# Performance work log

Hardware: AMD Instinct MI355X
Metric: run time of the kernel (lower is better)

Reference implementation:

```python
import jax, jax.numpy as jnp
import numpy as np

B, T, P = 4, 512, 3584          # batch, new tokens per seq, cached tokens per seq
D_MODEL, H, KH, DH = 2048, 16, 4, 128
N_REP = H // KH
MAX_SEQ = 4096
ROPE_BASE = 1e6
EPS = 1e-6


def _rmsnorm(t, w):
    # t: [..., DH]
    var = jnp.mean(t * t, axis=-1, keepdims=True)
    return t * jax.lax.rsqrt(var + EPS) * w


def _rope(t, positions):
    # t: [N, heads, DH], positions: [N] int
    half = DH // 2
    inv_freq = (1.0 / ROPE_BASE) ** (2.0 * jnp.arange(half, dtype=jnp.float32) / DH)
    theta = positions.astype(jnp.float32)[:, None] * inv_freq[None, :]   # [N, half]
    theta = jnp.concatenate([theta, theta], axis=-1)                      # [N, DH]
    sin = jnp.sin(theta)[:, None, :]
    cos = jnp.cos(theta)[:, None, :]
    x1, x2 = jnp.split(t, 2, axis=-1)
    rot = jnp.concatenate([-x2, x1], axis=-1)
    return cos * t + sin * rot


def setup_inputs() -> dict:
    key = jax.random.key(0)
    ks = jax.random.split(key, 9)
    N = B * T
    x = jax.random.normal(ks[0], (N, D_MODEL), dtype=jnp.float32)
    k_cache = jax.random.normal(ks[1], (B, KH, P, DH), dtype=jnp.float32)
    v_cache = jax.random.normal(ks[2], (B, KH, P, DH), dtype=jnp.float32)
    s = 1.0 / np.sqrt(D_MODEL)
    w_q = jax.random.normal(ks[3], (H * DH, D_MODEL), dtype=jnp.float32) * s
    w_k = jax.random.normal(ks[4], (KH * DH, D_MODEL), dtype=jnp.float32) * s
    w_v = jax.random.normal(ks[5], (KH * DH, D_MODEL), dtype=jnp.float32) * s
    w_o = jax.random.normal(ks[6], (D_MODEL, H * DH), dtype=jnp.float32) * s
    q_norm_w = jnp.ones((DH,), dtype=jnp.float32)
    k_norm_w = jnp.ones((DH,), dtype=jnp.float32)
    # each sequence's new tokens occupy absolute positions [P, P+T)
    positions = jnp.tile(P + jnp.arange(T, dtype=jnp.int32), B)  # [B*T]
    return {"x": x, "k_cache": k_cache, "v_cache": v_cache,
            "w_q": w_q, "w_k": w_k, "w_v": w_v, "w_o": w_o,
            "q_norm_w": q_norm_w, "k_norm_w": k_norm_w,
            "positions": positions}


def reference(x, k_cache, v_cache, w_q, w_k, w_v, w_o, q_norm_w, k_norm_w, positions):
    N = x.shape[0]
    # QKV projections (no bias)
    q = (x @ w_q.T).reshape(N, H, DH)
    k = (x @ w_k.T).reshape(N, KH, DH)
    v = (x @ w_v.T).reshape(N, KH, DH)
    # per-head RMSNorm then RoPE at absolute positions
    q = _rope(_rmsnorm(q, q_norm_w), positions)
    k = _rope(_rmsnorm(k, k_norm_w), positions)
    # assemble full KV: cached (pre-rotated) past + new tokens
    k_new = k.reshape(B, T, KH, DH).transpose(0, 2, 1, 3)   # [B,KH,T,DH]
    v_new = v.reshape(B, T, KH, DH).transpose(0, 2, 1, 3)
    k_full = jnp.concatenate([k_cache, k_new], axis=2)       # [B,KH,P+T,DH]
    v_full = jnp.concatenate([v_cache, v_new], axis=2)
    # GQA: repeat each kv head n_rep times
    k_rep = jnp.repeat(k_full, N_REP, axis=1)                # [B,H,S,DH]
    v_rep = jnp.repeat(v_full, N_REP, axis=1)
    q4 = q.reshape(B, T, H, DH).transpose(0, 2, 1, 3)        # [B,H,T,DH]
    scale = 1.0 / jnp.sqrt(jnp.float32(DH))
    scores = jnp.einsum('bhtd,bhsd->bhts', q4, k_rep) * scale  # [B,H,T,P+T]
    # right-bottom causal mask: q_pos = P + t, kv_pos = s
    q_pos = P + jnp.arange(T)
    kv_pos = jnp.arange(P + T)
    mask = q_pos[:, None] >= kv_pos[None, :]
    scores = jnp.where(mask[None, None], scores, -jnp.inf)
    attn = jax.nn.softmax(scores, axis=-1)
    out = jnp.einsum('bhts,bhsd->bhtd', attn, v_rep)          # [B,H,T,DH]
    out = out.transpose(0, 2, 1, 3).reshape(N, H * DH)
    return out @ w_o.T
```

## Files before the change

kernel.cpp:

```cpp
#include <hip/hip_runtime.h>
#include <hip/hip_bf16.h>
#include <stdint.h>

#define B_   4
#define T_   512
#define P_   3584
#define S_   4096
#define H_   16
#define KH_  4
#define DM_  2048
#define DH_  128
#define NTOK 2048
#define NCHUNK 3
#define NTC  43
#define NROWS 32768

typedef __attribute__((ext_vector_type(8)))  short          bf16x8;
typedef __attribute__((ext_vector_type(4)))  float          f32x4;
typedef __attribute__((ext_vector_type(16))) float          f32x16;
typedef __attribute__((ext_vector_type(4)))  float          f4v;
typedef __attribute__((ext_vector_type(4)))  unsigned short us4v;

__device__ __forceinline__ unsigned short f2bf(float x) {
    union { float f; unsigned u; } v; v.f = x;
    unsigned r = v.u + 0x7FFFu + ((v.u >> 16) & 1u);
    return (unsigned short)(r >> 16);
}
__device__ __forceinline__ float bf2f(unsigned short b) {
    union { unsigned u; float f; } v; v.u = ((unsigned)b) << 16; return v.f;
}
__device__ __forceinline__ unsigned pkbf(float a, float b) {
    __hip_bfloat162 h = __float22bfloat162_rn(float2{a, b});
    union { __hip_bfloat162 h; unsigned u; } cv; cv.h = h; return cv.u;
}

#define GLDS16(gp, lp) __builtin_amdgcn_global_load_lds( \
    (const __attribute__((address_space(1))) void*)(gp), \
    (__attribute__((address_space(3))) void*)(lp), 16, 0, 0)

__global__ __launch_bounds__(256) void convert_all(
    const float* __restrict__ x,  const float* __restrict__ wq,
    const float* __restrict__ wk, const float* __restrict__ wv,
    const float* __restrict__ wo, const float* __restrict__ kc,
    unsigned short* __restrict__ xb,   unsigned short* __restrict__ wqkvb,
    unsigned short* __restrict__ wob,  unsigned short* __restrict__ kfull)
{
    const long total = 5505024;
    for (long i = (long)blockIdx.x * 256 + threadIdx.x; i < total;
         i += (long)gridDim.x * 256) {
        const f4v* src; us4v* dst; long s4, d4;
        if (i < 1048576)      { src=(const f4v*)x;  dst=(us4v*)xb;              s4=i;         d4=s4; }
        else if (i < 2097152) { src=(const f4v*)wq; dst=(us4v*)wqkvb;           s4=i-1048576; d4=s4; }
        else if (i < 2359296) { src=(const f4v*)wk; dst=(us4v*)(wqkvb+4194304); s4=i-2097152; d4=s4; }
        else if (i < 2621440) { src=(const f4v*)wv; dst=(us4v*)(wqkvb+5242880); s4=i-2359296; d4=s4; }
        else if (i < 3670016) { src=(const f4v*)wo; dst=(us4v*)wob;             s4=i-2621440; d4=s4; }
        else                  { s4=i-3670016; long bk=s4/114688;
                                d4=bk*131072+(s4-bk*114688);
                                src=(const f4v*)kc; dst=(us4v*)kfull; }
        f4v v = src[s4];
        us4v o; o[0]=f2bf(v[0]); o[1]=f2bf(v[1]); o[2]=f2bf(v[2]); o[3]=f2bf(v[3]);
        dst[d4] = o;
    }
}

__global__ __launch_bounds__(256) void vcache_transpose(
    const float* __restrict__ vc, unsigned short* __restrict__ vT)
{
    __shared__ unsigned short tile[64][65];
    const int bk = blockIdx.z;
    const int st = blockIdx.x;
    const int dt = blockIdx.y;
    const float* src = vc + ((size_t)bk * P_ + st * 64) * DH_ + dt * 64;
    const int tq = threadIdx.x & 15;
    const int ts = threadIdx.x >> 4;
    #pragma unroll
    for (int i = 0; i < 4; ++i) {
        const int si = ts + i * 16;
        f4v v = *(const f4v*)(src + (size_t)si * DH_ + tq * 4);
        tile[si][tq*4+0] = f2bf(v[0]); tile[si][tq*4+1] = f2bf(v[1]);
        tile[si][tq*4+2] = f2bf(v[2]); tile[si][tq*4+3] = f2bf(v[3]);
    }
    __syncthreads();
    unsigned short* dst = vT + ((size_t)bk * DH_ + dt * 64) * S_ + st * 64;
    const int sq = threadIdx.x & 15;
    const int td = threadIdx.x >> 4;
    #pragma unroll
    for (int i = 0; i < 4; ++i) {
        const int di = td + i * 16;
        us4v o;
        o[0] = tile[sq*4+0][di]; o[1] = tile[sq*4+1][di];
        o[2] = tile[sq*4+2][di]; o[3] = tile[sq*4+3][di];
        *(us4v*)(dst + (size_t)di * S_ + sq * 4) = o;
    }
}

__global__ __launch_bounds__(256) void gemm_bt(
    const unsigned short* __restrict__ A, const unsigned short* __restrict__ Bw,
    void* __restrict__ C, int M, int N, int K, int obf16)
{
    __shared__ short As[2][128 * 32];
    __shared__ short Bs[2][128 * 32];
    const int tid = threadIdx.x, lane = tid & 63, w = tid >> 6;
    const int nbn = N >> 7;
    const int bm = blockIdx.x / nbn, bn = blockIdx.x % nbn;
    const int m0 = bm << 7, n0 = bn << 7;
    const int wm = w >> 1, wn = w & 1;

    f32x4 acc[4][4];
    #pragma unroll
    for (int i = 0; i < 4; ++i)
        #pragma unroll
        for (int j = 0; j < 4; ++j)
            #pragma unroll
            for (int r = 0; r < 4; ++r) acc[i][j][r] = 0.f;

    const int arow = lane >> 2;
    const int acol = (lane & 3) << 3;

    auto stage = [&](int buf, int k0) {
        #pragma unroll
        for (int cc = 0; cc < 2; ++cc) {
            const int c = 2 * w + cc;
            GLDS16(A  + (size_t)(m0 + c * 16 + arow) * K + k0 + acol, &As[buf][c * 512]);
            GLDS16(Bw + (size_t)(n0 + c * 16 + arow) * K + k0 + acol, &Bs[buf][c * 512]);
        }
    };

    stage(0, 0);
    __syncthreads();

    const int nk = K >> 5;
    const int fr = lane & 15, fk = (lane >> 4) << 3;
    for (int t = 0; t < nk; ++t) {
        const int buf = t & 1;
        if (t + 1 < nk) stage(buf ^ 1, (t + 1) << 5);
        bf16x8 a[4], b[4];
        #pragma unroll
        for (int i = 0; i < 4; ++i)
            a[i] = *(const bf16x8*)&As[buf][(wm * 64 + i * 16 + fr) * 32 + fk];
        #pragma unroll
        for (int j = 0; j < 4; ++j)
            b[j] = *(const bf16x8*)&Bs[buf][(wn * 64 + j * 16 + fr) * 32 + fk];
        #pragma unroll
        for (int i = 0; i < 4; ++i)
            #pragma unroll
            for (int j = 0; j < 4; ++j)
                acc[i][j] = __builtin_amdgcn_mfma_f32_16x16x32_bf16(a[i], b[j], acc[i][j], 0, 0, 0);
        __syncthreads();
    }

    const int er = lane >> 4, ec = lane & 15;
    #pragma unroll
    for (int i = 0; i < 4; ++i)
        #pragma unroll
        for (int j = 0; j < 4; ++j)
            #pragma unroll
            for (int r = 0; r < 4; ++r) {
                const int row = m0 + wm * 64 + i * 16 + er * 4 + r;
                const int col = n0 + wn * 64 + j * 16 + ec;
                if (obf16) ((unsigned short*)C)[(size_t)row * N + col] = f2bf(acc[i][j][r]);
                else       ((float*)C)[(size_t)row * N + col] = acc[i][j][r];
            }
}

__global__ __launch_bounds__(64) void norm_rope(
    const unsigned short* __restrict__ qkv, const float* __restrict__ qw,
    const float* __restrict__ kw,  const int* __restrict__ pos,
    unsigned short* __restrict__ Qb, unsigned short* __restrict__ Kf,
    unsigned short* __restrict__ VT)
{
    const int task = blockIdx.x;
    const int n = task / 24, idx = task % 24;
    const int lane = threadIdx.x;
    const int b = n >> 9, t = n & 511;

    if (idx >= 20) {
        const int kh = idx - 20;
        const unsigned short* src = qkv + (size_t)n * 3072 + 2560 + kh * 128;
        unsigned short* dstT = VT + (size_t)(b * KH_ + kh) * DH_ * S_ + (P_ + t);
        dstT[(size_t)lane * S_]        = src[lane];
        dstT[(size_t)(lane + 64) * S_] = src[lane + 64];
        return;
    }
    const bool isq = idx < 16;
    const int hh = isq ? idx : (idx - 16);
    const unsigned short* src = qkv + (size_t)n * 3072 + (isq ? hh * 128 : 2048 + hh * 128);
    const float* wn_ = isq ? qw : kw;
    float x0 = bf2f(src[lane]), x1 = bf2f(src[lane + 64]);
    float ss = x0 * x0 + x1 * x1;
    #pragma unroll
    for (int m = 1; m < 64; m <<= 1) ss += __shfl_xor(ss, m);
    const float rinv = rsqrtf(ss * (1.0f / 128.0f) + 1e-6f);
    float y0 = x0 * rinv * wn_[lane];
    float y1 = x1 * rinv * wn_[lane + 64];
    const float fr = __expf(-(float)lane * (13.815510557964274f / 64.0f));
    const float th = (float)pos[n] * fr;
    float sn, cs; sincosf(th, &sn, &cs);
    float o0 = cs * y0 - sn * y1;
    float o1 = cs * y1 + sn * y0;
    unsigned short* dst;
    if (isq) {
        o0 *= 0.08838834764831845f; o1 *= 0.08838834764831845f;
        dst = Qb + ((size_t)(b * H_ + hh) * T_ + t) * DH_;
    } else {
        dst = Kf + ((size_t)(b * KH_ + hh) * S_ + P_ + t) * DH_;
    }
    dst[lane]      = f2bf(o0);
    dst[lane + 64] = f2bf(o1);
}

__global__ __launch_bounds__(256, 3) void attn(
    const unsigned short* __restrict__ Qb, const unsigned short* __restrict__ Kf,
    const unsigned short* __restrict__ VT, unsigned short* __restrict__ op0,
    unsigned short* __restrict__ op1, unsigned short* __restrict__ op2,
    float2* __restrict__ ml)
{
    __shared__ short Ks[2][32 * 128];
    __shared__ short Vs[2][128 * 32];

    const int tid = threadIdx.x, lane = tid & 63, w = tid >> 6;
    const int c = blockIdx.x >> 8;
    const int rest = blockIdx.x & 255;
    const int qt = rest & 3;
    const int bh = rest >> 2;
    const int h = bh & 15, b = bh >> 4;
    const int kvh = h >> 2;
    const int t0 = qt * 128;

    const unsigned short* Qrow = Qb + (size_t)(b * H_ + h) * T_ * DH_;
    const unsigned short* Kb   = Kf + (size_t)(b * KH_ + kvh) * S_ * DH_;
    const unsigned short* VTb  = VT + (size_t)(b * KH_ + kvh) * DH_ * S_;

    const int ql = lane & 31;
    const int hi = lane >> 5;

    bf16x8 qf[8];
    {
        const unsigned short* qp = Qrow + (size_t)(t0 + w * 32 + ql) * DH_ + hi * 8;
        #pragma unroll
        for (int d0 = 0; d0 < 8; ++d0) qf[d0] = *(const bf16x8*)(qp + d0 * 16);
    }

    f32x16 o[4];
    #pragma unroll
    for (int d = 0; d < 4; ++d)
        #pragma unroll
        for (int r = 0; r < 16; ++r) o[d][r] = 0.f;
    float m_run = -INFINITY, l_run = 0.f;

    const int q_pos = P_ + t0 + w * 32 + ql;
    const int s_end_wave = P_ + t0 + w * 32 + 32;
    const int nt_full = (P_ + t0 + 128) >> 5;
    const int tstart = c * NTC;
    const int tend = min(tstart + NTC, nt_full);

    auto stage = [&](int buf, int tile) {
        const int s0 = tile << 5;
        #pragma unroll
        for (int cc = 0; cc < 2; ++cc) {
            const int cx = 2 * w + cc;
            const int krow = cx * 4 + (lane >> 4);
            const int kel  = 8 * ((lane & 15) ^ (krow & 15));
            GLDS16(Kb + (size_t)(s0 + krow) * DH_ + kel, &Ks[buf][cx * 512]);
            const int vrow = cx * 16 + (lane >> 2);
            const int vel  = 8 * ((lane & 3) ^ ((lane >> 3) & 3));
            GLDS16(VTb + (size_t)vrow * S_ + s0 + vel, &Vs[buf][cx * 512]);
        }
    };

    stage(0, tstart);
    __syncthreads();

    for (int i = 0, t = tstart; t < tend; ++t, ++i) {
        const int buf = i & 1;
        const int s0 = t << 5;
        if (t + 1 < tend) stage(buf ^ 1, t + 1);
        if (s0 < s_end_wave) {
            f32x16 st;
            #pragma unroll
            for (int r = 0; r < 16; ++r) st[r] = 0.f;
            {
                const char* kbase = (const char*)&Ks[buf][0] + ql * 256;
                const int sw = 16 * (ql & 15);
                #pragma unroll
                for (int d0 = 0; d0 < 8; ++d0) {
                    bf16x8 kfr = *(const bf16x8*)(kbase + ((d0 * 32 + 16 * hi) ^ sw));
                    st = __builtin_amdgcn_mfma_f32_32x32x16_bf16(kfr, qf[d0], st, 0, 0, 0);
                }
            }
            if (s0 + 31 > P_ + t0 + w * 32) {
                #pragma unroll
                for (int r = 0; r < 16; ++r) {
                    const int srow = (r & 3) + 8 * (r >> 2) + 4 * hi;
                    if (s0 + srow > q_pos) st[r] = -INFINITY;
                }
            }
            float pmax = st[0];
            #pragma unroll
            for (int r = 1; r < 16; ++r) pmax = fmaxf(pmax, st[r]);
            pmax = fmaxf(pmax, __shfl_xor(pmax, 32));
            if (!__all(pmax <= m_run + 8.f)) {
                const float m_new = fmaxf(m_run, pmax);
                const float alpha = __expf(m_run - m_new);
                l_run *= alpha;
                #pragma unroll
                for (int r = 0; r < 16; ++r) {
                    const int qr = (r & 3) + 8 * (r >> 2) + 4 * hi;
                    const float a = __shfl(alpha, qr);
                    #pragma unroll
                    for (int d = 0; d < 4; ++d) o[d][r] *= a;
                }
                m_run = m_new;
            }
            float p[16]; float psum = 0.f;
            #pragma unroll
            for (int r = 0; r < 16; ++r) { p[r] = __expf(st[r] - m_run); psum += p[r]; }
            psum += __shfl_xor(psum, 32);
            l_run += psum;
            unsigned pk[8];
            #pragma unroll
            for (int u = 0; u < 8; ++u) pk[u] = pkbf(p[2 * u], p[2 * u + 1]);
            unsigned xw[8];
            #pragma unroll
            for (int u = 0; u < 8; ++u) xw[u] = (unsigned)__shfl_xor((int)pk[u], 32);
            union { bf16x8 v; unsigned u[4]; } pa0, pa1;
            pa0.u[0] = hi ? xw[2] : pk[0];  pa0.u[1] = hi ? xw[3] : pk[1];
            pa0.u[2] = hi ? pk[2] : xw[0];  pa0.u[3] = hi ? pk[3] : xw[1];
            pa1.u[0] = hi ? xw[6] : pk[4];  pa1.u[1] = hi ? xw[7] : pk[5];
            pa1.u[2] = hi ? pk[6] : xw[4];  pa1.u[3] = hi ? pk[7] : xw[5];
            #pragma unroll
            for (int ch = 0; ch < 2; ++ch)
                #pragma unroll
                for (int db = 0; db < 4; ++db) {
                    const int vrow = db * 32 + ql;
                    bf16x8 vf = *(const bf16x8*)&Vs[buf][vrow * 32 + 8 * ((2 * ch + hi) ^ ((ql >> 1) & 3))];
                    o[db] = __builtin_amdgcn_mfma_f32_32x32x16_bf16(
                        ch ? pa1.v : pa0.v, vf, o[db], 0, 0, 0);
                }
        }
        __syncthreads();
    }

    unsigned short* op = (c == 0) ? op0 : (c == 1) ? op1 : op2;
    const int rowbase = (b * H_ + h) * T_ + t0 + w * 32;
    if (hi == 0) ml[c * NROWS + rowbase + ql] = float2{m_run, l_run};
    #pragma unroll
    for (int r = 0; r < 16; ++r) {
        const int qr = (r & 3) + 8 * (r >> 2) + 4 * hi;
        unsigned short* orow = op + (size_t)(rowbase + qr) * DH_;
        #pragma unroll
        for (int d = 0; d < 4; ++d)
            orow[d * 32 + ql] = f2bf(o[d][r]);
    }
}

__global__ __launch_bounds__(256) void combine(
    const float2* __restrict__ ml,
    const unsigned short* __restrict__ op0, const unsigned short* __restrict__ op1,
    const unsigned short* __restrict__ op2, unsigned short* __restrict__ ao)
{
    const int row = blockIdx.x * 4 + (threadIdx.x >> 6);
    const int lane = threadIdx.x & 63;
    const float2 a0 = ml[row], a1 = ml[NROWS + row], a2 = ml[2 * NROWS + row];
    const float m = fmaxf(a0.x, fmaxf(a1.x, a2.x));
    const float w0 = __expf(a0.x - m), w1 = __expf(a1.x - m), w2 = __expf(a2.x - m);
    const float Linv = 1.0f / (w0 * a0.y + w1 * a1.y + w2 * a2.y);
    const size_t src = (size_t)row * DH_ + 2 * lane;
    const unsigned u0 = *(const unsigned*)(op0 + src);
    const unsigned u1 = *(const unsigned*)(op1 + src);
    const unsigned u2 = *(const unsigned*)(op2 + src);
    const float v0 = (bf2f((unsigned short)u0) * w0 + bf2f((unsigned short)u1) * w1 +
                      bf2f((unsigned short)u2) * w2) * Linv;
    const float v1 = (bf2f((unsigned short)(u0 >> 16)) * w0 + bf2f((unsigned short)(u1 >> 16)) * w1 +
                      bf2f((unsigned short)(u2 >> 16)) * w2) * Linv;
    const int t = row & 511, h = (row >> 9) & 15, b = row >> 13;
    unsigned short* dst = ao + ((size_t)(b * T_ + t) * (H_ * DH_)) + h * DH_ + 2 * lane;
    *(unsigned*)dst = pkbf(v0, v1);
}

extern "C" void kernel_launch(void* const* d_in, const int* in_sizes, int n_in,
                              void* d_out, int out_size, void* d_ws, size_t ws_size,
                              hipStream_t stream)
{
    const float* x   = (const float*)d_in[0];
    const float* kc  = (const float*)d_in[1];
    const float* vc  = (const float*)d_in[2];
    const float* wq  = (const float*)d_in[3];
    const float* wk  = (const float*)d_in[4];
    const float* wv  = (const float*)d_in[5];
    const float* wo  = (const float*)d_in[6];
    const float* qnw = (const float*)d_in[7];
    const float* knw = (const float*)d_in[8];
    const int*   pos = (const int*)d_in[9];
    float* out = (float*)d_out;

    char* ws = (char*)d_ws;
    unsigned short* xb    = (unsigned short*)(ws + 0);
    unsigned short* wqkvb = (unsigned short*)(ws + 8388608);
    unsigned short* wob   = (unsigned short*)(ws + 20971520);
    unsigned short* qkvb  = (unsigned short*)(ws + 29360128);
    unsigned short* qb    = (unsigned short*)(ws + 41943040);
    unsigned short* kfull = (unsigned short*)(ws + 50331648);
    unsigned short* vT    = (unsigned short*)(ws + 67108864);
    unsigned short* ao    = (unsigned short*)(ws + 83886080);
    unsigned short* op0   = (unsigned short*)(ws + 0);
    unsigned short* op1   = (unsigned short*)(ws + 8388608);
    float2*         ml    = (float2*)(ws + 16777216);
    unsigned short* op2   = (unsigned short*)(ws + 29360128);

    hipLaunchKernelGGL(convert_all, dim3(2048), dim3(256), 0, stream,
                       x, wq, wk, wv, wo, kc, xb, wqkvb, wob, kfull);
    hipLaunchKernelGGL(vcache_transpose, dim3(P_ / 64, 2, B_ * KH_), dim3(256), 0, stream,
                       vc, vT);
    hipLaunchKernelGGL(gemm_bt, dim3(16 * 24), dim3(256), 0, stream,
                       xb, wqkvb, (void*)qkvb, 2048, 3072, 2048, 1);
    hipLaunchKernelGGL(norm_rope, dim3(NTOK * 24), dim3(64), 0, stream,
                       qkvb, qnw, knw, pos, qb, kfull, vT);
    hipLaunchKernelGGL(attn, dim3(NCHUNK * 256), dim3(256), 0, stream,
                       qb, kfull, vT, op0, op1, op2, ml);
    hipLaunchKernelGGL(combine, dim3(NROWS / 4), dim3(256), 0, stream,
                       ml, op0, op1, op2, ao);
    hipLaunchKernelGGL(gemm_bt, dim3(16 * 16), dim3(256), 0, stream,
                       ao, wob, (void*)out, 2048, 2048, 2048, 0);
}
```

Baseline: 233.8 us.

## Use base-2 exp softmax, XCD-aware attention block mapping, and batched norm_rope

The Q scale now folds in log2(e), so softmax, rescaling and combine call the raw v_exp_f32 instruction instead of __expf, and the lazy-rescale threshold is widened to match base-2 units. RoPE uses hardware v_sin/v_cos on a range-reduced revolution count instead of sincosf. The row max uses v_max3. Attention blocks are remapped so that blocks sharing a KV head land on the same XCD, which should improve L2 reuse of K/V. norm_rope packs four wavefront tasks per 256-thread block to cut block launch overhead. Hardware sin/cos at large angles lose some precision, and the wider threshold permits larger unnormalized exponents before a rescale.

```diff
diff --git a/kernel.cpp b/kernel.cpp
--- a/kernel.cpp
+++ b/kernel.cpp
@@ -32,6 +32,18 @@
 __device__ __forceinline__ unsigned pkbf(float a, float b) {
     __hip_bfloat162 h = __float22bfloat162_rn(float2{a, b});
     union { __hip_bfloat162 h; unsigned u; } cv; cv.h = h; return cv.u;
+}
+__device__ __forceinline__ float ex2(float x) {
+    float r; asm("v_exp_f32 %0, %1" : "=v"(r) : "v"(x)); return r;
+}
+__device__ __forceinline__ float max3f(float a, float b, float c) {
+    float r; asm("v_max3_f32 %0, %1, %2, %3" : "=v"(r) : "v"(a), "v"(b), "v"(c)); return r;
+}
+__device__ __forceinline__ float sin_rev(float xf) {
+    float r; asm("v_sin_f32 %0, %1" : "=v"(r) : "v"(xf)); return r;
+}
+__device__ __forceinline__ float cos_rev(float xf) {
+    float r; asm("v_cos_f32 %0, %1" : "=v"(r) : "v"(xf)); return r;
 }
 
 #define GLDS16(gp, lp) __builtin_amdgcn_global_load_lds( \
@@ -163,15 +175,15 @@
             }
 }
 
-__global__ __launch_bounds__(64) void norm_rope(
+__global__ __launch_bounds__(256) void norm_rope(
     const unsigned short* __restrict__ qkv, const float* __restrict__ qw,
     const float* __restrict__ kw,  const int* __restrict__ pos,
     unsigned short* __restrict__ Qb, unsigned short* __restrict__ Kf,
     unsigned short* __restrict__ VT)
 {
-    const int task = blockIdx.x;
+    const int task = blockIdx.x * 4 + (threadIdx.x >> 6);
     const int n = task / 24, idx = task % 24;
-    const int lane = threadIdx.x;
+    const int lane = threadIdx.x & 63;
     const int b = n >> 9, t = n & 511;
 
     if (idx >= 20) {
@@ -193,14 +205,17 @@
     const float rinv = rsqrtf(ss * (1.0f / 128.0f) + 1e-6f);
     float y0 = x0 * rinv * wn_[lane];
     float y1 = x1 * rinv * wn_[lane + 64];
-    const float fr = __expf(-(float)lane * (13.815510557964274f / 64.0f));
+    const float fr = ex2(-(float)lane * (19.931568569324174f / 64.0f));
     const float th = (float)pos[n] * fr;
-    float sn, cs; sincosf(th, &sn, &cs);
+    const float xr = th * 0.15915494309189535f;
+    const float xf = xr - floorf(xr);
+    const float sn = sin_rev(xf), cs = cos_rev(xf);
     float o0 = cs * y0 - sn * y1;
     float o1 = cs * y1 + sn * y0;
     unsigned short* dst;
     if (isq) {
-        o0 *= 0.08838834764831845f; o1 *= 0.08838834764831845f;
+        const float qs = 0.08838834764831845f * 1.4426950408889634f;
+        o0 *= qs; o1 *= qs;
         dst = Qb + ((size_t)(b * H_ + hh) * T_ + t) * DH_;
     } else {
         dst = Kf + ((size_t)(b * KH_ + hh) * S_ + P_ + t) * DH_;
@@ -220,11 +235,13 @@
 
     const int tid = threadIdx.x, lane = tid & 63, w = tid >> 6;
     const int c = blockIdx.x >> 8;
-    const int rest = blockIdx.x & 255;
-    const int qt = rest & 3;
-    const int bh = rest >> 2;
-    const int h = bh & 15, b = bh >> 4;
-    const int kvh = h >> 2;
+    const int y = blockIdx.x & 255;
+    const int xcd = y & 7, slot = y >> 3;
+    const int p = xcd + 8 * (slot >> 4);
+    const int inner = slot & 15;
+    const int b = p >> 2, kvh = p & 3;
+    const int h = kvh * 4 + (inner >> 2);
+    const int qt = inner & 3;
     const int t0 = qt * 128;
 
     const unsigned short* Qrow = Qb + (size_t)(b * H_ + h) * T_ * DH_;
@@ -295,13 +312,14 @@
                     if (s0 + srow > q_pos) st[r] = -INFINITY;
                 }
             }
-            float pmax = st[0];
-            #pragma unroll
-            for (int r = 1; r < 16; ++r) pmax = fmaxf(pmax, st[r]);
+            float m0_ = max3f(st[0], st[1], st[2]),  m1_ = max3f(st[3], st[4], st[5]);
+            float m2_ = max3f(st[6], st[7], st[8]),  m3_ = max3f(st[9], st[10], st[11]);
+            float m4_ = max3f(st[12], st[13], st[14]);
+            float pmax = fmaxf(max3f(m0_, m1_, m2_), max3f(m3_, m4_, st[15]));
             pmax = fmaxf(pmax, __shfl_xor(pmax, 32));
-            if (!__all(pmax <= m_run + 8.f)) {
+            if (!__all(pmax <= m_run + 11.5f)) {
                 const float m_new = fmaxf(m_run, pmax);
-                const float alpha = __expf(m_run - m_new);
+                const float alpha = ex2(m_run - m_new);
                 l_run *= alpha;
                 #pragma unroll
                 for (int r = 0; r < 16; ++r) {
@@ -312,14 +330,14 @@
                 }
                 m_run = m_new;
             }
-            float p[16]; float psum = 0.f;
-            #pragma unroll
-            for (int r = 0; r < 16; ++r) { p[r] = __expf(st[r] - m_run); psum += p[r]; }
+            float pv[16]; float psum = 0.f;
+            #pragma unroll
+            for (int r = 0; r < 16; ++r) { pv[r] = ex2(st[r] - m_run); psum += pv[r]; }
             psum += __shfl_xor(psum, 32);
             l_run += psum;
             unsigned pk[8];
             #pragma unroll
-            for (int u = 0; u < 8; ++u) pk[u] = pkbf(p[2 * u], p[2 * u + 1]);
+            for (int u = 0; u < 8; ++u) pk[u] = pkbf(pv[2 * u], pv[2 * u + 1]);
             unsigned xw[8];
             #pragma unroll
             for (int u = 0; u < 8; ++u) xw[u] = (unsigned)__shfl_xor((int)pk[u], 32);
@@ -363,7 +381,7 @@
     const int lane = threadIdx.x & 63;
     const float2 a0 = ml[row], a1 = ml[NROWS + row], a2 = ml[2 * NROWS + row];
     const float m = fmaxf(a0.x, fmaxf(a1.x, a2.x));
-    const float w0 = __expf(a0.x - m), w1 = __expf(a1.x - m), w2 = __expf(a2.x - m);
+    const float w0 = ex2(a0.x - m), w1 = ex2(a1.x - m), w2 = ex2(a2.x - m);
     const float Linv = 1.0f / (w0 * a0.y + w1 * a1.y + w2 * a2.y);
     const size_t src = (size_t)row * DH_ + 2 * lane;
     const unsigned u0 = *(const unsigned*)(op0 + src);
@@ -414,7 +432,7 @@
                        vc, vT);
     hipLaunchKernelGGL(gemm_bt, dim3(16 * 24), dim3(256), 0, stream,
                        xb, wqkvb, (void*)qkvb, 2048, 3072, 2048, 1);
-    hipLaunchKernelGGL(norm_rope, dim3(NTOK * 24), dim3(64), 0, stream,
+    hipLaunchKernelGGL(norm_rope, dim3(NTOK * 24 / 4), dim3(256), 0, stream,
                        qkvb, qnw, knw, pos, qb, kfull, vT);
     hipLaunchKernelGGL(attn, dim3(NCHUNK * 256), dim3(256), 0, stream,
                        qb, kfull, vT, op0, op1, op2, ml);
```

After: 230.9 us. About the same (-1.2%).
